# Kernel tuning notes

Measured on AMD Instinct MI355X. Metric: run time of the kernel, lower is better.

Reference implementation:

```python
import jax, jax.numpy as jnp
import numpy as np

MAX_H = 22
NUM_HEADS = 8
EPS = 1e-5
SLOPE = 0.01  # torch LeakyReLU default


def setup_inputs() -> dict:
    key = jax.random.key(0)
    ks = jax.random.split(key, 8)
    n, c, s, h, w = 16, 64, 30, 64, 22
    cp, v = 64, 17
    p, out_c = 7, 256
    D = c * MAX_H + cp * 2  # fuse_dim = 1536
    sil = jax.random.normal(ks[0], (n, c, s, h, w), dtype=jnp.float32)
    pose = jax.random.normal(ks[1], (n, cp, s, v), dtype=jnp.float32)
    min_idx = jax.random.randint(ks[2], (p, n), 0, h - MAX_H + 1, dtype=jnp.int32)
    max_idx = min_idx + MAX_H  # slices are exactly MAX_H rows (static shape)
    fc_bin = jax.random.normal(ks[3], (p, D, out_c), dtype=jnp.float32) * np.sqrt(2.0 / (D + out_c))
    gamma = 1.0 + 0.1 * jax.random.normal(ks[4], (out_c,), dtype=jnp.float32)
    beta = 0.1 * jax.random.normal(ks[5], (out_c,), dtype=jnp.float32)
    w_qkv = jax.random.normal(ks[6], (3 * out_c, out_c), dtype=jnp.float32) * 0.02
    w_proj = jax.random.normal(ks[7], (out_c, out_c), dtype=jnp.float32) * 0.02
    return {"sil": sil, "pose": pose, "fc_bin": fc_bin, "gamma": gamma, "beta": beta,
            "w_qkv": w_qkv, "w_proj": w_proj, "min_idx": min_idx, "max_idx": max_idx}


def _forward(sil, pose, fc_bin, gamma, beta, w_qkv, w_proj, min_idx):
    n, c, s, h, w = sil.shape
    p = min_idx.shape[0]
    sil_p = jnp.transpose(sil, (0, 2, 1, 3, 4))  # [n,s,c,h,w]
    parts = []
    for j in range(p):  # fixed small part loop; each gather is a big vectorized op
        idx = min_idx[j][:, None] + jnp.arange(MAX_H, dtype=min_idx.dtype)  # [n,MAX_H]
        g = jnp.take_along_axis(sil_p, idx[:, None, None, :, None], axis=3)  # [n,s,c,MAX_H,w]
        parts.append(g.mean(-1) + g.max(-1))  # mean + max pool over width
    silpart = jnp.stack(parts, 0)  # [p,n,s,c,MAX_H]
    silpart = jnp.transpose(silpart, (1, 2, 0, 3, 4)).reshape(n * s, p, c * MAX_H)

    cp, v = pose.shape[1], pose.shape[3]
    pose_r = jnp.transpose(pose, (0, 2, 1, 3)).reshape(n * s, cp, v)  # [ns,cp,17]
    # part 0: AdaptiveAvgPool1d(2) on 5 joints -> mean(j0..j2), mean(j2..j4)
    part0 = jnp.stack([pose_r[:, :, 0:3].mean(-1), pose_r[:, :, 2:5].mean(-1)], -1)  # [ns,cp,2]
    # parts 1..6: pairs of joints, pool(2->2) is identity
    others = pose_r[:, :, 5:].reshape(n * s, cp, 6, 2).transpose(0, 2, 1, 3)  # [ns,6,cp,2]
    posepart = jnp.concatenate([part0[:, None], others], axis=1)  # [ns,p,cp,2]
    posepart = jax.nn.leaky_relu(posepart, SLOPE).reshape(n * s, p, cp * 2)

    fuse = jnp.concatenate([silpart, posepart], axis=2)  # [ns,p,D]
    x = jnp.einsum('npd,pdo->npo', fuse, fc_bin)  # per-part FC -> [ns,p,out]

    # BatchNorm1d (training-mode batch stats) over [ns,out,p]
    x = jnp.transpose(x, (0, 2, 1))  # [ns,out,p]
    mu = x.mean((0, 2), keepdims=True)
    var = x.var((0, 2), keepdims=True)
    x = (x - mu) * jax.lax.rsqrt(var + EPS) * gamma[None, :, None] + beta[None, :, None]
    x = jnp.transpose(x, (0, 2, 1))  # [ns,p,out]

    # Attention over the p part tokens (note: source softmaxes over the HEAD axis)
    B, N, C = x.shape
    hd = C // NUM_HEADS
    qkv = (x @ w_qkv.T).reshape(B, N, 3, NUM_HEADS, hd).transpose(2, 0, 3, 1, 4)
    q, k, vv = qkv[0], qkv[1], qkv[2]  # [B,H,N,hd]
    attn = jnp.einsum('bhnd,bhmd->bhnm', q, k) * (hd ** -0.5)
    attn = jax.nn.softmax(attn, axis=1)  # faithful to attn.softmax(dim=1)
    ao = jnp.einsum('bhnm,bhmd->bhnd', attn, vv).transpose(0, 2, 1, 3).reshape(B, N, C)
    x = x + ao @ w_proj.T

    return x.reshape(n, s, p, C).transpose(0, 3, 1, 2)  # [n,out,s,p]


def reference(sil, pose, fc_bin, gamma, beta, w_qkv, w_proj, min_idx, max_idx):
    # max_idx == min_idx + MAX_H by construction; slice length is static MAX_H
    return _forward(sil, pose, fc_bin, gamma, beta, w_qkv, w_proj, min_idx)
```

## Files before the change

### kernel.cpp

```cpp
#include <hip/hip_runtime.h>
#include <hip/hip_bf16.h>
#include <math.h>

#define NS 480
#define NN 16
#define SS 30
#define CC 64
#define HHH 64
#define WW 22
#define PP 7
#define MAXH 22
#define CP 64
#define VV 17
#define DD 1536
#define OC 256
#define SILD 1408
#define NTOK 3360

typedef __bf16 bf16x8 __attribute__((ext_vector_type(8)));
typedef float f32x4 __attribute__((ext_vector_type(4)));
typedef short short8 __attribute__((ext_vector_type(8)));

__device__ __forceinline__ void gl_lds16(const void* g, void* l) {
    __builtin_amdgcn_global_load_lds(
        (const __attribute__((address_space(1))) void*)g,
        (__attribute__((address_space(3))) void*)l, 16, 0, 0);
}

__device__ __forceinline__ float bf2f(short s) {
    union { float f; unsigned u; } uu; uu.u = ((unsigned)(unsigned short)s) << 16; return uu.f;
}

__global__ __launch_bounds__(256) void prep(const float* __restrict__ sil,
                                            const int* __restrict__ min_idx,
                                            const float* __restrict__ wqkv,
                                            const float* __restrict__ wproj,
                                            const float* __restrict__ fcbin,
                                            const float* __restrict__ pose,
                                            __hip_bfloat16* __restrict__ fuse,
                                            __hip_bfloat16* __restrict__ wqkv16,
                                            __hip_bfloat16* __restrict__ wproj16,
                                            __hip_bfloat16* __restrict__ fcbinT16) {
    __shared__ __align__(16) char smem[47552];
    int b = blockIdx.x, tid = threadIdx.x;
    if (b < 3840) {
        float* lds  = (float*)smem;
        float* hbuf = (float*)(smem + 45056);
        int*   mi_s = (int*)(smem + 47104);
        if (tid < 112) mi_s[tid] = min_idx[tid];
        long long base = (long long)b * 11264;
        int w = tid >> 6, lane = tid & 63;
        const char* gsrc = (const char*)(sil + base) + lane * 16;
        #pragma unroll
        for (int i = 0; i < 11; i++) {
            int ci = w * 11 + i;
            gl_lds16(gsrc + ci * 1024, (char*)smem + ci * 1024);
        }
        __syncthreads();
        #pragma unroll
        for (int rr = 0; rr < 2; rr++) {
            int r = tid + rr * 256;
            const float* row = lds + r * 22;
            float s = 0.f, m = -INFINITY;
            #pragma unroll
            for (int k = 0; k < WW; k++) { float v = row[k]; s += v; m = fmaxf(m, v); }
            hbuf[r] = s * (1.0f / WW) + m;
        }
        __syncthreads();
        int q0 = b * 8;
        for (int idx = tid; idx < 8 * PP * MAXH; idx += 256) {
            int hh = idx % MAXH;
            int t2 = idx / MAXH;
            int j = t2 % PP, qi = t2 / PP;
            int q = q0 + qi;
            int s_i = q % SS, t3 = q / SS;
            int c = t3 & 63, n = t3 >> 6;
            int mi = mi_s[j * NN + n];
            fuse[((long long)(j * NS + n * SS + s_i)) * DD + c * MAXH + hh] =
                __float2bfloat16(hbuf[qi * 64 + mi + hh]);
        }
        return;
    }
    b -= 3840;
    if (b < 768)  { int g = b * 256 + tid; wqkv16[g] = __float2bfloat16(wqkv[g]); return; }
    if (b < 1024) { int g = (b - 768) * 256 + tid; wproj16[g] = __float2bfloat16(wproj[g]); return; }
    if (b < 1696) {
        float (*t)[65] = (float(*)[65])smem;
        int bb = b - 1024;
        int p = bb / 96, r2 = bb % 96, dt = r2 / 4, ot = r2 % 4;
        const float* s = fcbin + ((long long)p * DD + dt * 64) * OC + ot * 64;
        for (int i = tid; i < 64 * 64; i += 256) {
            int r = i >> 6, c = i & 63;
            t[r][c] = s[(long long)r * OC + c];
        }
        __syncthreads();
        __hip_bfloat16* d = fcbinT16 + ((long long)p * OC + ot * 64) * DD + dt * 64;
        for (int i = tid; i < 64 * 64; i += 256) {
            int r = i >> 6, c = i & 63;
            d[(long long)r * DD + c] = __float2bfloat16(t[c][r]);
        }
        return;
    }
    int g = (b - 1696) * 256 + tid;
    int dd = g & 127;
    int t2 = g >> 7;
    int nsi = t2 % NS;
    int j = t2 / NS;
    int n = nsi / SS, s_i = nsi % SS;
    int cpi = dd >> 1, par = dd & 1;
    const float* pr = pose + (((long long)n * CP + cpi) * SS + s_i) * VV;
    float v;
    if (j == 0) {
        v = (par == 0) ? (pr[0] + pr[1] + pr[2]) * (1.f / 3.f)
                       : (pr[2] + pr[3] + pr[4]) * (1.f / 3.f);
    } else {
        v = pr[5 + (j - 1) * 2 + par];
    }
    v = (v > 0.f) ? v : 0.01f * v;
    fuse[(long long)(j * NS + nsi) * DD + SILD + dd] = __float2bfloat16(v);
}

__global__ __launch_bounds__(512) void gemm_fc(
    const __hip_bfloat16* __restrict__ Ain, const __hip_bfloat16* __restrict__ Bt,
    float* __restrict__ Cf, float* __restrict__ partial)
{
    const int M = 480, K = 1536, lda = 1536, ldc = 1792;
    const __hip_bfloat16* Ab = Ain + (long long)blockIdx.z * 480 * 1536;
    const __hip_bfloat16* Bq = Bt + (long long)blockIdx.z * 256 * 1536;
    float* C = Cf + (long long)blockIdx.z * 256;

    __shared__ short As[2][2][4096];
    __shared__ short Bs[2][2][4096];
    __shared__ float red[4][2][16][2];

    int tid = threadIdx.x, lane = tid & 63, w = tid >> 6;
    int kg = w >> 2, wq = w & 3;
    int wm = wq >> 1, wn = wq & 1;
    int row0 = blockIdx.x * 64, col0 = blockIdx.y * 64;
    int kbase = kg * 768;

    f32x4 acc[2][2] = {};

    auto stage = [&](int buf, int k0) {
        int cc = lane & 7;
        #pragma unroll
        for (int i = 0; i < 2; i++) {
            int r = wq * 16 + i * 8 + (lane >> 3);
            int grow = row0 + r; if (grow >= M) grow = M - 1;
            long long kk = kbase + k0;
            const char* ga = (const char*)Ab + (((long long)grow * lda + kk) << 1) + ((cc ^ (r & 7)) << 4);
            gl_lds16(ga, (char*)&As[kg][buf][0] + (wq * 16 + i * 8) * 128);
            const char* gb = (const char*)Bq + (((long long)(col0 + r) * K + kk) << 1) + ((cc ^ (r & 7)) << 4);
            gl_lds16(gb, (char*)&Bs[kg][buf][0] + (wq * 16 + i * 8) * 128);
        }
    };

    stage(0, 0);
    __syncthreads();
    for (int t = 0; t < 12; t++) {
        int cur = t & 1;
        if (t + 1 < 12) stage(cur ^ 1, (t + 1) << 6);
        #pragma unroll
        for (int ks = 0; ks < 2; ks++) {
            bf16x8 af[2], bfv[2];
            #pragma unroll
            for (int f = 0; f < 2; f++) {
                int r = wm * 32 + f * 16 + (lane & 15);
                int ca = (ks * 4 + (lane >> 4)) ^ (r & 7);
                af[f] = *(const bf16x8*)((const char*)&As[kg][cur][0] + r * 128 + (ca << 4));
                int rb = wn * 32 + f * 16 + (lane & 15);
                int cb = (ks * 4 + (lane >> 4)) ^ (rb & 7);
                bfv[f] = *(const bf16x8*)((const char*)&Bs[kg][cur][0] + rb * 128 + (cb << 4));
            }
            #pragma unroll
            for (int fm = 0; fm < 2; fm++)
                #pragma unroll
                for (int fn = 0; fn < 2; fn++)
                    acc[fm][fn] = __builtin_amdgcn_mfma_f32_16x16x32_bf16(
                        af[fm], bfv[fn], acc[fm][fn], 0, 0, 0);
        }
        __syncthreads();
    }

    float* redC = (float*)&As[0][0][0];
    if (kg == 1) {
        #pragma unroll
        for (int fm = 0; fm < 2; fm++)
            #pragma unroll
            for (int fn = 0; fn < 2; fn++)
                #pragma unroll
                for (int r4 = 0; r4 < 4; r4++) {
                    int rl = wm * 32 + fm * 16 + (lane >> 4) * 4 + r4;
                    int cl = wn * 32 + fn * 16 + (lane & 15);
                    redC[rl * 64 + cl] = acc[fm][fn][r4];
                }
    }
    __syncthreads();

    if (kg == 0) {
        float s[2] = {0.f, 0.f}, s2[2] = {0.f, 0.f};
        #pragma unroll
        for (int fm = 0; fm < 2; fm++) {
            #pragma unroll
            for (int fn = 0; fn < 2; fn++) {
                #pragma unroll
                for (int r4 = 0; r4 < 4; r4++) {
                    int rl = wm * 32 + fm * 16 + (lane >> 4) * 4 + r4;
                    int cl = wn * 32 + fn * 16 + (lane & 15);
                    int grow = row0 + rl;
                    if (grow < M) {
                        float v = acc[fm][fn][r4] + redC[rl * 64 + cl];
                        C[(long long)grow * ldc + col0 + cl] = v;
                        s[fn] += v; s2[fn] += v * v;
                    }
                }
            }
        }
        #pragma unroll
        for (int off = 16; off < 64; off <<= 1) {
            s[0] += __shfl_xor(s[0], off);  s2[0] += __shfl_xor(s2[0], off);
            s[1] += __shfl_xor(s[1], off);  s2[1] += __shfl_xor(s2[1], off);
        }
        if (lane < 16) {
            red[wq][0][lane][0] = s[0]; red[wq][0][lane][1] = s2[0];
            red[wq][1][lane][0] = s[1]; red[wq][1][lane][1] = s2[1];
        }
    }
    __syncthreads();
    if (tid < 128) {
        int col = tid >> 1, which = tid & 1;
        int wn2 = (col >> 5) & 1, fn2 = (col >> 4) & 1, c16 = col & 15;
        float v = red[wn2][fn2][c16][which] + red[2 + wn2][fn2][c16][which];
        partial[((long long)(blockIdx.z * 8 + blockIdx.x) * 2 + which) * 256 + blockIdx.y * 64 + col] = v;
    }
}

__global__ __launch_bounds__(256) void qkvattn(const float* __restrict__ xraw,
                                               const __hip_bfloat16* __restrict__ wqkv16,
                                               const __hip_bfloat16* __restrict__ wproj16,
                                               const float* __restrict__ partial,
                                               const float* __restrict__ gamma,
                                               const float* __restrict__ beta,
                                               float* __restrict__ outp) {
    __shared__ short As[16 * 256];
    __shared__ float qkvs[7 * 768];
    __shared__ float as_[8][49];
    __shared__ short ao_s[16 * 256];
    __shared__ float Ct[256 * 9];
    __shared__ float ssl[512];

    int tid = threadIdx.x, lane = tid & 63, w = tid >> 6;
    int token0 = blockIdx.x * 7;

    {
        float s = 0.f, s2 = 0.f;
        #pragma unroll 8
        for (int bb = 0; bb < 56; bb++) {
            s  += partial[bb * 512 + tid];
            s2 += partial[bb * 512 + 256 + tid];
        }
        float mu = s * (1.f / NTOK);
        float var = s2 * (1.f / NTOK) - mu * mu;
        float rsig = rsqrtf(var + 1e-5f);
        float sc = gamma[tid] * rsig;
        ssl[tid] = sc;
        ssl[256 + tid] = beta[tid] - mu * sc;
    }
    __syncthreads();

    for (int i = tid; i < 512; i += 256) {
        int r = i >> 5, c8 = i & 31;
        short8 o = {};
        if (r < 7) {
            const float* src = xraw + (long long)(token0 + r) * 256 + c8 * 8;
            float4 v0 = *(const float4*)src;
            float4 v1 = *(const float4*)(src + 4);
            float vv[8] = {v0.x, v0.y, v0.z, v0.w, v1.x, v1.y, v1.z, v1.w};
            #pragma unroll
            for (int j2 = 0; j2 < 8; j2++) {
                float tv = vv[j2] * ssl[c8 * 8 + j2] + ssl[256 + c8 * 8 + j2];
                union { __hip_bfloat16 h; short s; } u; u.h = __float2bfloat16(tv);
                o[j2] = u.s;
            }
        }
        *(short8*)&As[r * 256 + ((c8 ^ (r & 7)) << 3)] = o;
    }
    __syncthreads();

    {
        f32x4 qacc[12] = {};
        int n0w = w * 192;
        #pragma unroll
        for (int k0 = 0; k0 < 256; k0 += 32) {
            int r = lane & 15;
            int kk = k0 + (lane >> 4) * 8;
            int ck = kk >> 3;
            bf16x8 af = *(const bf16x8*)(const void*)&As[r * 256 + ((ck ^ (r & 7)) << 3)];
            #pragma unroll
            for (int fn = 0; fn < 12; fn++) {
                int nn2 = n0w + fn * 16 + (lane & 15);
                bf16x8 bv = *(const bf16x8*)(const void*)((const short*)wqkv16 + nn2 * 256 + kk);
                qacc[fn] = __builtin_amdgcn_mfma_f32_16x16x32_bf16(af, bv, qacc[fn], 0, 0, 0);
            }
        }
        #pragma unroll
        for (int fn = 0; fn < 12; fn++)
            #pragma unroll
            for (int r4 = 0; r4 < 4; r4++) {
                int row = (lane >> 4) * 4 + r4;
                if (row < 7) qkvs[row * 768 + n0w + fn * 16 + (lane & 15)] = qacc[fn][r4];
            }
    }
    __syncthreads();

    for (int t = tid; t < 392; t += 256) {
        int h = t / 49, ij = t % 49, i = ij / 7, j = ij % 7;
        const float* qp = qkvs + i * 768 + h * 32;
        const float* kp = qkvs + j * 768 + 256 + h * 32;
        float acc = 0.f;
        #pragma unroll
        for (int d = 0; d < 32; d++) acc += qp[d] * kp[d];
        as_[h][ij] = acc * 0.17677669529663689f;
    }
    __syncthreads();
    if (tid < 49) {
        float m = -INFINITY;
        #pragma unroll
        for (int h = 0; h < 8; h++) m = fmaxf(m, as_[h][tid]);
        float e[8], sum = 0.f;
        #pragma unroll
        for (int h = 0; h < 8; h++) { e[h] = __expf(as_[h][tid] - m); sum += e[h]; }
        float inv = 1.f / sum;
        #pragma unroll
        for (int h = 0; h < 8; h++) as_[h][tid] = e[h] * inv;
    }
    __syncthreads();
    #pragma unroll
    for (int it = 0; it < 16; it++) {
        int tl = it, col = tid;
        float acc = 0.f;
        if (tl < 7) {
            int h = col >> 5;
            const float* ap = &as_[h][tl * 7];
            const float* vp = qkvs + 512 + col;
            #pragma unroll
            for (int j = 0; j < 7; j++) acc += ap[j] * vp[j * 768];
        }
        int c16 = col >> 3;
        union { __hip_bfloat16 h2; short s2; } u; u.h2 = __float2bfloat16(acc);
        ao_s[tl * 256 + ((c16 ^ (tl & 7)) << 3) + (col & 7)] = u.s2;
    }
    __syncthreads();
    f32x4 pacc[4] = {};
    int n0 = w * 64;
    #pragma unroll
    for (int k0 = 0; k0 < 256; k0 += 32) {
        int rowa = lane & 15;
        int kk = k0 + (lane >> 4) * 8;
        int c16a = kk >> 3;
        bf16x8 af = *(const bf16x8*)(const void*)&ao_s[rowa * 256 + ((c16a ^ (rowa & 7)) << 3)];
        #pragma unroll
        for (int fn = 0; fn < 4; fn++) {
            int n = n0 + fn * 16 + (lane & 15);
            bf16x8 bfv = *(const bf16x8*)(const void*)((const short*)wproj16 + n * 256 + kk);
            pacc[fn] = __builtin_amdgcn_mfma_f32_16x16x32_bf16(af, bfv, pacc[fn], 0, 0, 0);
        }
    }
    #pragma unroll
    for (int fn = 0; fn < 4; fn++)
        #pragma unroll
        for (int r4 = 0; r4 < 4; r4++) {
            int tk = (lane >> 4) * 4 + r4;
            if (tk < 7) {
                int o = n0 + fn * 16 + (lane & 15);
                Ct[o * 9 + tk] = pacc[fn][r4];
            }
        }
    __syncthreads();
    int o = tid;
    int n = token0 / 210, rem0 = token0 % 210;
    float* op = outp + ((long long)(n * 256 + o)) * 210 + rem0;
    float sc = ssl[o], sh = ssl[256 + o];
    #pragma unroll
    for (int tk = 0; tk < 7; tk++) {
        op[tk] = Ct[o * 9 + tk] + xraw[(long long)(token0 + tk) * 256 + o] * sc + sh;
    }
}

extern "C" void kernel_launch(void* const* d_in, const int* in_sizes, int n_in,
                              void* d_out, int out_size, void* d_ws, size_t ws_size,
                              hipStream_t stream) {
    const float* sil   = (const float*)d_in[0];
    const float* pose  = (const float*)d_in[1];
    const float* fcbin = (const float*)d_in[2];
    const float* gamma = (const float*)d_in[3];
    const float* beta  = (const float*)d_in[4];
    const float* wqkv  = (const float*)d_in[5];
    const float* wproj = (const float*)d_in[6];
    const int*   minidx= (const int*)d_in[7];
    float* out = (float*)d_out;

    float* ws = (float*)d_ws;
    __hip_bfloat16* fuse16   = (__hip_bfloat16*)ws;
    float* xraw    = ws + 2580480;
    float* partial = ws + 3440640;
    __hip_bfloat16* wqkv16   = (__hip_bfloat16*)(ws + 3469312);
    __hip_bfloat16* wproj16  = (__hip_bfloat16*)(ws + 3567616);
    __hip_bfloat16* fcbinT16 = (__hip_bfloat16*)(ws + 3600384);

    prep<<<7216, 256, 0, stream>>>(sil, minidx, wqkv, wproj, fcbin, pose,
                                   fuse16, wqkv16, wproj16, fcbinT16);
    gemm_fc<<<dim3(8, 4, 7), 512, 0, stream>>>(fuse16, fcbinT16, xraw, partial);
    qkvattn<<<480, 256, 0, stream>>>(xraw, wqkv16, wproj16, partial, gamma, beta, out);
}
```

Baseline: 93.31 us.

## Split QKV projection into a tiled GEMM kernel and separate BN finalize

The fused per-7-token attention kernel is split into three kernels. A single-block kernel finalizes the batch-norm statistics, a 64x64-tiled double-buffered MFMA GEMM computes QKV for all tokens into a bf16 buffer, and a slimmer attention and projection kernel reads that buffer. The old kernel used only 7 of 16 MFMA rows and streamed the full QKV weight from global memory per block. The split keeps weight tiles in LDS and removes the 56-block partial reduction that each of the 480 blocks repeated. In exchange it adds two kernel launches, a round trip of the QKV intermediate through global memory, and an extra bf16 rounding of QKV.

```diff
diff --git a/kernel.cpp b/kernel.cpp
--- a/kernel.cpp
+++ b/kernel.cpp
@@ -16,6 +16,7 @@
 #define OC 256
 #define SILD 1408
 #define NTOK 3360
+#define LDQ 776
 
 typedef __bf16 bf16x8 __attribute__((ext_vector_type(8)));
 typedef float f32x4 __attribute__((ext_vector_type(4)));
@@ -235,88 +236,142 @@
     }
 }
 
-__global__ __launch_bounds__(256) void qkvattn(const float* __restrict__ xraw,
-                                               const __hip_bfloat16* __restrict__ wqkv16,
-                                               const __hip_bfloat16* __restrict__ wproj16,
-                                               const float* __restrict__ partial,
+__global__ __launch_bounds__(256) void bnfinal(const float* __restrict__ partial,
                                                const float* __restrict__ gamma,
                                                const float* __restrict__ beta,
-                                               float* __restrict__ outp) {
-    __shared__ short As[16 * 256];
-    __shared__ float qkvs[7 * 768];
-    __shared__ float as_[8][49];
-    __shared__ short ao_s[16 * 256];
-    __shared__ float Ct[256 * 9];
+                                               float* __restrict__ ssbuf) {
+    int t = threadIdx.x;
+    float s = 0.f, s2 = 0.f;
+    #pragma unroll 8
+    for (int b = 0; b < 56; b++) { s += partial[b * 512 + t]; s2 += partial[b * 512 + 256 + t]; }
+    float mu = s / (float)NTOK;
+    float var = s2 / (float)NTOK - mu * mu;
+    float rsig = rsqrtf(var + 1e-5f);
+    float sc = gamma[t] * rsig;
+    ssbuf[t] = sc;
+    ssbuf[256 + t] = beta[t] - mu * sc;
+}
+
+__global__ __launch_bounds__(256) void gemm_qkv(
+    const float* __restrict__ xraw, const __hip_bfloat16* __restrict__ Bt,
+    const float* __restrict__ ssb, __hip_bfloat16* __restrict__ qkv16)
+{
+    const int M = 3360, K = 256;
+    __shared__ short As[2][4096];
+    __shared__ short Bs[2][4096];
     __shared__ float ssl[512];
+    int tid = threadIdx.x, lane = tid & 63, w = tid >> 6;
+    int wm = w >> 1, wn = w & 1;
+    int row0 = blockIdx.x * 64, col0 = blockIdx.y * 64;
+
+    for (int i = tid; i < 512; i += 256) ssl[i] = ssb[i];
+    __syncthreads();
+
+    f32x4 acc[2][2] = {};
+
+    auto stageB = [&](int buf, int k0) {
+        int cc = lane & 7;
+        #pragma unroll
+        for (int i = 0; i < 2; i++) {
+            int r = w * 16 + i * 8 + (lane >> 3);
+            const char* gb = (const char*)Bt + (((long long)(col0 + r) * K + k0) << 1) + ((cc ^ (r & 7)) << 4);
+            gl_lds16(gb, (char*)&Bs[buf][0] + (w * 16 + i * 8) * 128);
+        }
+    };
+    auto stageA = [&](int buf, int k0) {
+        #pragma unroll
+        for (int i = 0; i < 2; i++) {
+            int id = tid + i * 256;
+            int r = id >> 3, c8 = id & 7;
+            int grow = row0 + r; if (grow >= M) grow = M - 1;
+            const float* src = xraw + (long long)grow * 256 + k0 + c8 * 8;
+            float4 v0 = *(const float4*)src;
+            float4 v1 = *(const float4*)(src + 4);
+            int kb = k0 + c8 * 8;
+            float vv[8] = {v0.x, v0.y, v0.z, v0.w, v1.x, v1.y, v1.z, v1.w};
+            short8 o;
+            #pragma unroll
+            for (int j = 0; j < 8; j++) {
+                float tv = vv[j] * ssl[kb + j] + ssl[256 + kb + j];
+                union { __hip_bfloat16 h; short s; } u; u.h = __float2bfloat16(tv);
+                o[j] = u.s;
+            }
+            *(short8*)((char*)&As[buf][0] + r * 128 + ((c8 ^ (r & 7)) << 4)) = o;
+        }
+    };
+
+    stageA(0, 0); stageB(0, 0);
+    __syncthreads();
+    for (int t = 0; t < 4; t++) {
+        int cur = t & 1;
+        if (t + 1 < 4) { stageA(cur ^ 1, (t + 1) << 6); stageB(cur ^ 1, (t + 1) << 6); }
+        #pragma unroll
+        for (int ks = 0; ks < 2; ks++) {
+            bf16x8 af[2], bfv[2];
+            #pragma unroll
+            for (int f = 0; f < 2; f++) {
+                int r = wm * 32 + f * 16 + (lane & 15);
+                int ca = (ks * 4 + (lane >> 4)) ^ (r & 7);
+                af[f] = *(const bf16x8*)((const char*)&As[cur][0] + r * 128 + (ca << 4));
+                int rb = wn * 32 + f * 16 + (lane & 15);
+                int cb = (ks * 4 + (lane >> 4)) ^ (rb & 7);
+                bfv[f] = *(const bf16x8*)((const char*)&Bs[cur][0] + rb * 128 + (cb << 4));
+            }
+            #pragma unroll
+            for (int fm = 0; fm < 2; fm++)
+                #pragma unroll
+                for (int fn = 0; fn < 2; fn++)
+                    acc[fm][fn] = __builtin_amdgcn_mfma_f32_16x16x32_bf16(
+                        af[fm], bfv[fn], acc[fm][fn], 0, 0, 0);
+        }
+        __syncthreads();
+    }
+    #pragma unroll
+    for (int fm = 0; fm < 2; fm++)
+        #pragma unroll
+        for (int fn = 0; fn < 2; fn++)
+            #pragma unroll
+            for (int r4 = 0; r4 < 4; r4++) {
+                int grow = row0 + wm * 32 + fm * 16 + (lane >> 4) * 4 + r4;
+                int gcol = col0 + wn * 32 + fn * 16 + (lane & 15);
+                if (grow < M)
+                    qkv16[(long long)grow * 768 + gcol] = __float2bfloat16(acc[fm][fn][r4]);
+            }
+}
+
+__global__ __launch_bounds__(256) void attnproj(const __hip_bfloat16* __restrict__ qkv16,
+                                                const __hip_bfloat16* __restrict__ wproj16,
+                                                const float* __restrict__ xraw,
+                                                const float* __restrict__ ssb,
+                                                float* __restrict__ outp) {
+    __shared__ __align__(16) char sm[33728];
+    float* qkvs = (float*)sm;
+    float* Ct   = (float*)sm;
+    short* ao_s = (short*)(sm + 21728);
+    float (*as_)[49] = (float(*)[49])(sm + 29920);
+    float* ssl  = (float*)(sm + 31680);
 
     int tid = threadIdx.x, lane = tid & 63, w = tid >> 6;
     int token0 = blockIdx.x * 7;
 
-    {
-        float s = 0.f, s2 = 0.f;
-        #pragma unroll 8
-        for (int bb = 0; bb < 56; bb++) {
-            s  += partial[bb * 512 + tid];
-            s2 += partial[bb * 512 + 256 + tid];
-        }
-        float mu = s * (1.f / NTOK);
-        float var = s2 * (1.f / NTOK) - mu * mu;
-        float rsig = rsqrtf(var + 1e-5f);
-        float sc = gamma[tid] * rsig;
-        ssl[tid] = sc;
-        ssl[256 + tid] = beta[tid] - mu * sc;
-    }
-    __syncthreads();
-
-    for (int i = tid; i < 512; i += 256) {
-        int r = i >> 5, c8 = i & 31;
-        short8 o = {};
-        if (r < 7) {
-            const float* src = xraw + (long long)(token0 + r) * 256 + c8 * 8;
-            float4 v0 = *(const float4*)src;
-            float4 v1 = *(const float4*)(src + 4);
-            float vv[8] = {v0.x, v0.y, v0.z, v0.w, v1.x, v1.y, v1.z, v1.w};
-            #pragma unroll
-            for (int j2 = 0; j2 < 8; j2++) {
-                float tv = vv[j2] * ssl[c8 * 8 + j2] + ssl[256 + c8 * 8 + j2];
-                union { __hip_bfloat16 h; short s; } u; u.h = __float2bfloat16(tv);
-                o[j2] = u.s;
-            }
-        }
-        *(short8*)&As[r * 256 + ((c8 ^ (r & 7)) << 3)] = o;
-    }
-    __syncthreads();
-
-    {
-        f32x4 qacc[12] = {};
-        int n0w = w * 192;
-        #pragma unroll
-        for (int k0 = 0; k0 < 256; k0 += 32) {
-            int r = lane & 15;
-            int kk = k0 + (lane >> 4) * 8;
-            int ck = kk >> 3;
-            bf16x8 af = *(const bf16x8*)(const void*)&As[r * 256 + ((ck ^ (r & 7)) << 3)];
-            #pragma unroll
-            for (int fn = 0; fn < 12; fn++) {
-                int nn2 = n0w + fn * 16 + (lane & 15);
-                bf16x8 bv = *(const bf16x8*)(const void*)((const short*)wqkv16 + nn2 * 256 + kk);
-                qacc[fn] = __builtin_amdgcn_mfma_f32_16x16x32_bf16(af, bv, qacc[fn], 0, 0, 0);
-            }
-        }
-        #pragma unroll
-        for (int fn = 0; fn < 12; fn++)
-            #pragma unroll
-            for (int r4 = 0; r4 < 4; r4++) {
-                int row = (lane >> 4) * 4 + r4;
-                if (row < 7) qkvs[row * 768 + n0w + fn * 16 + (lane & 15)] = qacc[fn][r4];
-            }
+    for (int i = tid; i < 512; i += 256) ssl[i] = ssb[i];
+
+    const short* src = (const short*)qkv16 + (long long)token0 * 768;
+    for (int c = tid; c < 672; c += 256) {
+        int r = c / 96, c8 = (c % 96) * 8;
+        short8 v = *(const short8*)(src + r * 768 + c8);
+        float4 f0, f1;
+        f0.x = bf2f(v[0]); f0.y = bf2f(v[1]); f0.z = bf2f(v[2]); f0.w = bf2f(v[3]);
+        f1.x = bf2f(v[4]); f1.y = bf2f(v[5]); f1.z = bf2f(v[6]); f1.w = bf2f(v[7]);
+        *(float4*)&qkvs[r * LDQ + c8] = f0;
+        *(float4*)&qkvs[r * LDQ + c8 + 4] = f1;
     }
     __syncthreads();
 
     for (int t = tid; t < 392; t += 256) {
         int h = t / 49, ij = t % 49, i = ij / 7, j = ij % 7;
-        const float* qp = qkvs + i * 768 + h * 32;
-        const float* kp = qkvs + j * 768 + 256 + h * 32;
+        const float* qp = qkvs + i * LDQ + h * 32;
+        const float* kp = qkvs + j * LDQ + 256 + h * 32;
         float acc = 0.f;
         #pragma unroll
         for (int d = 0; d < 32; d++) acc += qp[d] * kp[d];
@@ -336,15 +391,15 @@
     }
     __syncthreads();
     #pragma unroll
-    for (int it = 0; it < 16; it++) {
-        int tl = it, col = tid;
+    for (int tl = 0; tl < 16; tl++) {
+        int col = tid;
         float acc = 0.f;
         if (tl < 7) {
             int h = col >> 5;
             const float* ap = &as_[h][tl * 7];
             const float* vp = qkvs + 512 + col;
             #pragma unroll
-            for (int j = 0; j < 7; j++) acc += ap[j] * vp[j * 768];
+            for (int j = 0; j < 7; j++) acc += ap[j] * vp[j * LDQ];
         }
         int c16 = col >> 3;
         union { __hip_bfloat16 h2; short s2; } u; u.h2 = __float2bfloat16(acc);
@@ -366,6 +421,7 @@
             pacc[fn] = __builtin_amdgcn_mfma_f32_16x16x32_bf16(af, bfv, pacc[fn], 0, 0, 0);
         }
     }
+    __syncthreads();
     #pragma unroll
     for (int fn = 0; fn < 4; fn++)
         #pragma unroll
@@ -404,12 +460,16 @@
     __hip_bfloat16* fuse16   = (__hip_bfloat16*)ws;
     float* xraw    = ws + 2580480;
     float* partial = ws + 3440640;
-    __hip_bfloat16* wqkv16   = (__hip_bfloat16*)(ws + 3469312);
-    __hip_bfloat16* wproj16  = (__hip_bfloat16*)(ws + 3567616);
-    __hip_bfloat16* fcbinT16 = (__hip_bfloat16*)(ws + 3600384);
+    float* ssbuf   = ws + 3469312;
+    __hip_bfloat16* wqkv16   = (__hip_bfloat16*)(ws + 3469824);
+    __hip_bfloat16* wproj16  = (__hip_bfloat16*)(ws + 3568128);
+    __hip_bfloat16* fcbinT16 = (__hip_bfloat16*)(ws + 3600896);
+    __hip_bfloat16* qkv16    = (__hip_bfloat16*)(ws + 4977152);
 
     prep<<<7216, 256, 0, stream>>>(sil, minidx, wqkv, wproj, fcbin, pose,
                                    fuse16, wqkv16, wproj16, fcbinT16);
     gemm_fc<<<dim3(8, 4, 7), 512, 0, stream>>>(fuse16, fcbinT16, xraw, partial);
-    qkvattn<<<480, 256, 0, stream>>>(xraw, wqkv16, wproj16, partial, gamma, beta, out);
-}
+    bnfinal<<<1, 256, 0, stream>>>(partial, gamma, beta, ssbuf);
+    gemm_qkv<<<dim3(53, 12), 256, 0, stream>>>(xraw, wqkv16, ssbuf, qkv16);
+    attnproj<<<480, 256, 0, stream>>>(qkv16, wproj16, xraw, ssbuf, out);
+}
```

Result: faster. 81.43 us (-12.7%).
